# Kernel tuning notes

Measured on AMD Instinct MI355X. Metric: run time of the kernel, lower is better.

## Reference

```python
import jax, jax.numpy as jnp
import numpy as np

B, N, M = 16, 4096, 1024
IN_C, OUT_C, D = 6, 128, 64


def _gn(x, w, b, groups, eps=1e-5):
    # GroupNorm over (C//groups, L) per group; x: [B, C, L]
    Bb, C, L = x.shape
    xg = x.reshape(Bb, groups, C // groups, L)
    mu = xg.mean(axis=(2, 3), keepdims=True)
    var = xg.var(axis=(2, 3), keepdims=True)
    xn = ((xg - mu) * jax.lax.rsqrt(var + eps)).reshape(Bb, C, L)
    return xn * w[None, :, None] + b[None, :, None]


def _sa(xq, xkv, xyz_q, xyz_kv, qk_w, v_w, v_b, t_w, t_b, gn_w, gn_b, p_w, pg_w):
    # offset self-attention (PCT SA_Layer), q/k share weights
    pq = jnp.einsum('bcn,dc->bnd', xyz_q, p_w)              # [B,N,D]
    pk = jnp.einsum('bcm,dc->bdm', xyz_kv, pg_w)            # [B,D,M]
    q = jnp.einsum('bcn,dc->bnd', xq, qk_w) + pq            # [B,N,D]
    k = jnp.einsum('bcm,dc->bdm', xkv, qk_w) + pk           # [B,D,M]
    v = jnp.einsum('bcm,dc->bdm', xkv, v_w) + v_b[None, :, None] + pk
    attn = jax.nn.softmax(jnp.einsum('bnd,bdm->bnm', q, k), axis=-1)
    attn = attn / (1e-9 + attn.sum(axis=1, keepdims=True))  # L1 renorm over queries
    x_r = jnp.einsum('bnm,bdm->bnd', attn, v)               # [B,N,D]
    t = jnp.einsum('bnd,od->bon', q - x_r, t_w) + t_b[None, :, None]
    t = jax.nn.relu(_gn(t, gn_w, gn_b, 4))
    return jnp.swapaxes(q, 1, 2) + t                        # [B,D,N]


def _forward(x, x_global, xyz, xyz_global, conv1_w, gn1_w, gn1_b, conv2_w, gn2_w, gn2_b, sa_qk_w, sa_v_w, sa_v_b, sa_trans_w, sa_trans_b, sa_gn_w, sa_gn_b, sa_pos_w, sa_posG_w, fuse_w, fuse_gn_w, fuse_gn_b, convs1_w, convs1_b, gns1_w, gns1_b, convs2_w, convs2_b, gns2_w, gns2_b):
    h = jax.nn.relu(_gn(jnp.einsum('bcn,oc->bon', x, conv1_w), gn1_w, gn1_b, 16))
    hg = jax.nn.relu(_gn(jnp.einsum('bcm,oc->bom', x_global, conv2_w), gn2_w, gn2_b, 16))
    outs = []
    cur = h
    for i in range(4):
        cur = _sa(cur, hg, xyz, xyz_global, sa_qk_w[i], sa_v_w[i], sa_v_b[i],
                  sa_trans_w[i], sa_trans_b[i], sa_gn_w[i], sa_gn_b[i],
                  sa_pos_w[i], sa_posG_w[i])
        outs.append(cur)
    xc = jnp.concatenate(outs, axis=1)                      # [B,4D,N]
    xf = jax.nn.leaky_relu(_gn(jnp.einsum('bcn,oc->bon', xc, fuse_w), fuse_gn_w, fuse_gn_b, 16), 0.2)
    s1 = jax.nn.relu(_gn(jnp.einsum('bcn,oc->bon', xf, convs1_w) + convs1_b[None, :, None], gns1_w, gns1_b, 8))
    # dropout is identity in eval mode
    s2 = jax.nn.relu(_gn(jnp.einsum('bcn,oc->bon', s1, convs2_w) + convs2_b[None, :, None], gns2_w, gns2_b, 4))
    return jnp.swapaxes(s2, 1, 2)                           # [B,N,OUT_C]


def setup_inputs() -> dict:
    ks = jax.random.split(jax.random.key(0), 16)
    f = lambda k, s, sc=0.1: jax.random.normal(k, s, dtype=jnp.float32) * sc
    return {
        'x': f(ks[0], (B, IN_C, N), 1.0),
        'x_global': f(ks[1], (B, 32, M), 1.0),
        'xyz': f(ks[2], (B, 3, N), 1.0),
        'xyz_global': f(ks[3], (B, 3, M), 1.0),
        'conv1_w': f(ks[4], (D, IN_C)),
        'gn1_w': jnp.ones((D,), jnp.float32), 'gn1_b': jnp.zeros((D,), jnp.float32),
        'conv2_w': f(ks[5], (D, 32)),
        'gn2_w': jnp.ones((D,), jnp.float32), 'gn2_b': jnp.zeros((D,), jnp.float32),
        'sa_qk_w': f(ks[6], (4, D, D)),
        'sa_v_w': f(ks[7], (4, D, D)),
        'sa_v_b': jnp.zeros((4, D), jnp.float32),
        'sa_trans_w': f(ks[8], (4, D, D)),
        'sa_trans_b': jnp.zeros((4, D), jnp.float32),
        'sa_gn_w': jnp.ones((4, D), jnp.float32), 'sa_gn_b': jnp.zeros((4, D), jnp.float32),
        'sa_pos_w': f(ks[9], (4, D, 3)),
        'sa_posG_w': f(ks[10], (4, D, 3)),
        'fuse_w': f(ks[11], (2 * D, 4 * D)),
        'fuse_gn_w': jnp.ones((2 * D,), jnp.float32), 'fuse_gn_b': jnp.zeros((2 * D,), jnp.float32),
        'convs1_w': f(ks[12], (512, 2 * D)),
        'convs1_b': jnp.zeros((512,), jnp.float32),
        'gns1_w': jnp.ones((512,), jnp.float32), 'gns1_b': jnp.zeros((512,), jnp.float32),
        'convs2_w': f(ks[13], (OUT_C, 512)),
        'convs2_b': jnp.zeros((OUT_C,), jnp.float32),
        'gns2_w': jnp.ones((OUT_C,), jnp.float32), 'gns2_b': jnp.zeros((OUT_C,), jnp.float32),
    }


def reference(x, x_global, xyz, xyz_global, conv1_w, gn1_w, gn1_b, conv2_w, gn2_w, gn2_b, sa_qk_w, sa_v_w, sa_v_b, sa_trans_w, sa_trans_b, sa_gn_w, sa_gn_b, sa_pos_w, sa_posG_w, fuse_w, fuse_gn_w, fuse_gn_b, convs1_w, convs1_b, gns1_w, gns1_b, convs2_w, convs2_b, gns2_w, gns2_b):
    return _forward(x, x_global, xyz, xyz_global, conv1_w, gn1_w, gn1_b, conv2_w, gn2_w, gn2_b, sa_qk_w, sa_v_w, sa_v_b, sa_trans_w, sa_trans_b, sa_gn_w, sa_gn_b, sa_pos_w, sa_posG_w, fuse_w, fuse_gn_w, fuse_gn_b, convs1_w, convs1_b, gns1_w, gns1_b, convs2_w, convs2_b, gns2_w, gns2_b)
```

## Files before the change

### kernel.cpp

```cpp
#include <hip/hip_runtime.h>
#include <hip/hip_bf16.h>

namespace {

constexpr int BB = 16;
constexpr int NN = 4096;
constexpr int MM = 1024;

using f32x4  = __attribute__((ext_vector_type(4))) float;
using bf16x8 = __attribute__((ext_vector_type(8))) short;

__device__ __forceinline__ float actf(float x, int act) {
    if (act == 1) return fmaxf(x, 0.f);
    if (act == 2) return x >= 0.f ? x : 0.2f * x;
    return x;
}

__device__ __forceinline__ ushort f2bf(float x) {
    __hip_bfloat16 h = __float2bfloat16(x);
    return *reinterpret_cast<ushort*>(&h);
}

__device__ __forceinline__ uint hilo_pack(float x) {
    ushort h = f2bf(x);
    float hf = __uint_as_float(((uint)h) << 16);
    ushort l = f2bf(x - hf);
    return (uint)h | ((uint)l << 16);
}

__device__ __forceinline__ void split8(const uint* d, bf16x8& hi, bf16x8& lo) {
    union { uint u[4]; bf16x8 v; } H, L;
#pragma unroll
    for (int j = 0; j < 4; ++j) {
        H.u[j] = (d[2 * j] & 0xffffu) | (d[2 * j + 1] << 16);
        L.u[j] = (d[2 * j] >> 16) | (d[2 * j + 1] & 0xffff0000u);
    }
    hi = H.v; lo = L.v;
}

__global__ __launch_bounds__(256)
void conv_mfma(const float* __restrict__ X, int C, long x_bs,
               const float* __restrict__ W,
               const float* __restrict__ X2, long x2_bs,
               const float* __restrict__ W2,
               const float* __restrict__ bias,
               float* __restrict__ Y, long y_bs, int L)
{
    __shared__ uint Wp[64 * 33];
    __shared__ uint Xp[128 * 33];
    const int t  = threadIdx.x;
    const int b  = blockIdx.z;
    const int o0 = blockIdx.y * 64;
    const int l0 = blockIdx.x * 128;
    const int w  = t >> 6;
    const int ln = t & 15;
    const int lq = (t >> 4) & 3;
    const int wo = (w & 1) * 32;
    const int wl = (w >> 1) * 64;
    const int sl  = t & 127;
    const int sch = (t >> 7) * 16;

    f32x4 acc[2][4];
#pragma unroll
    for (int i = 0; i < 2; ++i)
#pragma unroll
        for (int j = 0; j < 4; ++j) acc[i][j] = (f32x4){0.f, 0.f, 0.f, 0.f};

    for (int c0 = 0; c0 < C; c0 += 32) {
        __syncthreads();
#pragma unroll
        for (int i = 0; i < 2; ++i) {
            int f = i * 256 + t;
            int r = f >> 3, q4 = (f & 7) * 4;
            float4 wv = *reinterpret_cast<const float4*>(&W[(long)(o0 + r) * C + c0 + q4]);
            Wp[r * 33 + q4 + 0] = hilo_pack(wv.x);
            Wp[r * 33 + q4 + 1] = hilo_pack(wv.y);
            Wp[r * 33 + q4 + 2] = hilo_pack(wv.z);
            Wp[r * 33 + q4 + 3] = hilo_pack(wv.w);
        }
        {
            const float* xc = X + (long)b * x_bs + (long)(c0 + sch) * L + l0 + sl;
            uint tmp[16];
#pragma unroll
            for (int c = 0; c < 16; ++c) tmp[c] = hilo_pack(xc[(long)c * L]);
#pragma unroll
            for (int c4 = 0; c4 < 4; ++c4) {
                uint4 v = make_uint4(tmp[c4 * 4], tmp[c4 * 4 + 1],
                                     tmp[c4 * 4 + 2], tmp[c4 * 4 + 3]);
                *reinterpret_cast<uint4*>(&Xp[sl * 33 + sch + c4 * 4]) = v;
            }
        }
        __syncthreads();

        bf16x8 ahi[2], alo[2];
#pragma unroll
        for (int ot = 0; ot < 2; ++ot) {
            uint d[8];
            *reinterpret_cast<uint4*>(d) =
                *reinterpret_cast<const uint4*>(&Wp[(wo + ot * 16 + ln) * 33 + lq * 8]);
            *reinterpret_cast<uint4*>(d + 4) =
                *reinterpret_cast<const uint4*>(&Wp[(wo + ot * 16 + ln) * 33 + lq * 8 + 4]);
            split8(d, ahi[ot], alo[ot]);
        }
#pragma unroll
        for (int lt = 0; lt < 4; ++lt) {
            uint d[8];
            *reinterpret_cast<uint4*>(d) =
                *reinterpret_cast<const uint4*>(&Xp[(wl + lt * 16 + ln) * 33 + lq * 8]);
            *reinterpret_cast<uint4*>(d + 4) =
                *reinterpret_cast<const uint4*>(&Xp[(wl + lt * 16 + ln) * 33 + lq * 8 + 4]);
            bf16x8 bhi, blo;
            split8(d, bhi, blo);
#pragma unroll
            for (int ot = 0; ot < 2; ++ot) {
                acc[ot][lt] = __builtin_amdgcn_mfma_f32_16x16x32_bf16(alo[ot], bhi, acc[ot][lt], 0, 0, 0);
                acc[ot][lt] = __builtin_amdgcn_mfma_f32_16x16x32_bf16(ahi[ot], blo, acc[ot][lt], 0, 0, 0);
                acc[ot][lt] = __builtin_amdgcn_mfma_f32_16x16x32_bf16(ahi[ot], bhi, acc[ot][lt], 0, 0, 0);
            }
        }
    }

    float x2v[4][3];
    if (X2) {
#pragma unroll
        for (int lt = 0; lt < 4; ++lt) {
            const int l = l0 + wl + lt * 16 + ln;
#pragma unroll
            for (int c = 0; c < 3; ++c)
                x2v[lt][c] = X2[(long)b * x2_bs + (long)c * L + l];
        }
    }
#pragma unroll
    for (int ot = 0; ot < 2; ++ot)
#pragma unroll
        for (int r = 0; r < 4; ++r) {
            const int o = o0 + wo + ot * 16 + lq * 4 + r;
            float base = bias ? bias[o] : 0.f;
            float w20 = 0.f, w21 = 0.f, w22 = 0.f;
            if (X2) {
                w20 = W2[o * 3 + 0];
                w21 = W2[o * 3 + 1];
                w22 = W2[o * 3 + 2];
            }
#pragma unroll
            for (int lt = 0; lt < 4; ++lt) {
                const int l = l0 + wl + lt * 16 + ln;
                float val = acc[ot][lt][r] + base;
                if (X2)
                    val += w20 * x2v[lt][0] + w21 * x2v[lt][1] + w22 * x2v[lt][2];
                Y[(long)b * y_bs + (long)o * L + l] = val;
            }
        }
}

__global__ __launch_bounds__(256)
void conv_gemm(const float* __restrict__ X1, int C1, long x1_bs,
               const float* __restrict__ W1,
               const float* __restrict__ X2, int C2, long x2_bs,
               const float* __restrict__ W2,
               const float* __restrict__ bias,
               float* __restrict__ Y, long y_bs, int L)
{
    __shared__ float Wt[64][17];
    __shared__ float Xt[16][128];
    const int t  = threadIdx.x;
    const int b  = blockIdx.z;
    const int o0 = blockIdx.y * 64;
    const int l0 = blockIdx.x * 128;
    const int ty = t >> 4, tx = t & 15;

    float acc[4][8];
#pragma unroll
    for (int i = 0; i < 4; ++i)
#pragma unroll
        for (int j = 0; j < 8; ++j) acc[i][j] = 0.f;

    for (int pass = 0; pass < 2; ++pass) {
        const float* X = pass ? X2 : X1;
        const float* W = pass ? W2 : W1;
        const int    C = pass ? C2 : C1;
        const long xbs = pass ? x2_bs : x1_bs;
        if (C <= 0 || X == nullptr) continue;
        for (int c0 = 0; c0 < C; c0 += 16) {
            __syncthreads();
#pragma unroll
            for (int i = 0; i < 4; ++i) {
                int flat = i * 256 + t;
                int oo = flat >> 4, kk = flat & 15;
                Wt[oo][kk] = (c0 + kk < C) ? W[(long)(o0 + oo) * C + c0 + kk] : 0.f;
            }
#pragma unroll
            for (int i = 0; i < 2; ++i) {
                int f4 = i * 256 + t;
                int kk = f4 >> 5, c4 = f4 & 31;
                float4 xv = make_float4(0.f, 0.f, 0.f, 0.f);
                if (c0 + kk < C)
                    xv = *reinterpret_cast<const float4*>(
                        X + (long)b * xbs + (long)(c0 + kk) * L + l0 + c4 * 4);
                *reinterpret_cast<float4*>(&Xt[kk][c4 * 4]) = xv;
            }
            __syncthreads();
#pragma unroll
            for (int kk = 0; kk < 16; ++kk) {
                float wv[4];
#pragma unroll
                for (int i = 0; i < 4; ++i) wv[i] = Wt[ty * 4 + i][kk];
                float4 xa = *reinterpret_cast<const float4*>(&Xt[kk][tx * 8]);
                float4 xb = *reinterpret_cast<const float4*>(&Xt[kk][tx * 8 + 4]);
                float xv[8] = {xa.x, xa.y, xa.z, xa.w, xb.x, xb.y, xb.z, xb.w};
#pragma unroll
                for (int i = 0; i < 4; ++i)
#pragma unroll
                    for (int j = 0; j < 8; ++j) acc[i][j] += wv[i] * xv[j];
            }
        }
    }

#pragma unroll
    for (int i = 0; i < 4; ++i) {
        const int oo = o0 + ty * 4 + i;
        const float bv = bias ? bias[oo] : 0.f;
        float* yp = Y + (long)b * y_bs + (long)oo * L + l0 + tx * 8;
        float4 v0 = make_float4(acc[i][0] + bv, acc[i][1] + bv, acc[i][2] + bv, acc[i][3] + bv);
        float4 v1 = make_float4(acc[i][4] + bv, acc[i][5] + bv, acc[i][6] + bv, acc[i][7] + bv);
        *reinterpret_cast<float4*>(yp)     = v0;
        *reinterpret_cast<float4*>(yp + 4) = v1;
    }
}

__global__ __launch_bounds__(256)
void gn_stats(const float* __restrict__ Y, long y_bs, int cpg, int L, int G,
              float* __restrict__ stats)
{
    const int bg = blockIdx.x;
    const int b = bg / G, g = bg - b * G;
    const float* p = Y + (long)b * y_bs + (long)g * cpg * L;
    const long cnt = (long)cpg * L;
    float s = 0.f, ss = 0.f;
    for (long i = (long)threadIdx.x * 4; i < cnt; i += 256 * 4) {
        float4 v = *reinterpret_cast<const float4*>(p + i);
        s  += v.x + v.y + v.z + v.w;
        ss += v.x * v.x + v.y * v.y + v.z * v.z + v.w * v.w;
    }
    __shared__ float rs[256], rss[256];
    rs[threadIdx.x] = s; rss[threadIdx.x] = ss;
    __syncthreads();
    for (int st = 128; st > 0; st >>= 1) {
        if (threadIdx.x < st) {
            rs[threadIdx.x]  += rs[threadIdx.x + st];
            rss[threadIdx.x] += rss[threadIdx.x + st];
        }
        __syncthreads();
    }
    if (threadIdx.x == 0) {
        float mu  = rs[0] / (float)cnt;
        float var = rss[0] / (float)cnt - mu * mu;
        stats[bg * 2]     = mu;
        stats[bg * 2 + 1] = rsqrtf(var + 1e-5f);
    }
}

__global__ __launch_bounds__(256)
void gn_apply(const float* __restrict__ src, long s_bs,
              float* __restrict__ dst, long d_bs,
              const float* __restrict__ res, long r_bs,
              const float* __restrict__ w, const float* __restrict__ bb,
              const float* __restrict__ stats,
              int C, int cpg, int L, int act)
{
    const long total4 = (long)BB * C * L / 4;
    const int G = C / cpg;
    for (long i4 = (long)blockIdx.x * 256 + threadIdx.x; i4 < total4;
         i4 += (long)gridDim.x * 256) {
        long flat = i4 * 4;
        int b = (int)(flat / ((long)C * L));
        long rem = flat - (long)b * C * L;
        int c = (int)(rem / L);
        long li = rem - (long)c * L;
        int sidx = (b * G + c / cpg) * 2;
        float mu = stats[sidx], rsig = stats[sidx + 1];
        float sc = rsig * w[c];
        float sh = bb[c] - mu * sc;
        float4 vv = *reinterpret_cast<const float4*>(src + (long)b * s_bs + (long)c * L + li);
        float4 ov;
        ov.x = actf(vv.x * sc + sh, act);
        ov.y = actf(vv.y * sc + sh, act);
        ov.z = actf(vv.z * sc + sh, act);
        ov.w = actf(vv.w * sc + sh, act);
        if (res) {
            float4 rv = *reinterpret_cast<const float4*>(res + (long)b * r_bs + (long)c * L + li);
            ov.x += rv.x; ov.y += rv.y; ov.z += rv.z; ov.w += rv.w;
        }
        *reinterpret_cast<float4*>(dst + (long)b * d_bs + (long)c * L + li) = ov;
    }
}

__global__ __launch_bounds__(256)
void tcvt(const float* __restrict__ in, ushort* __restrict__ out, int L)
{
    __shared__ float ls[64][65];
    const int t = threadIdx.x, b = blockIdx.y;
    const int l0 = blockIdx.x * 64;
#pragma unroll
    for (int i = 0; i < 16; ++i) {
        int f = i * 256 + t;
        int d = f >> 6, l = f & 63;
        ls[d][l] = in[(long)b * 64 * L + (long)d * L + l0 + l];
    }
    __syncthreads();
#pragma unroll
    for (int i = 0; i < 16; ++i) {
        int f = i * 256 + t;
        int l = f >> 6, d = f & 63;
        out[((long)b * L + l0 + l) * 64 + d] = f2bf(ls[d][l]);
    }
}

__global__ __launch_bounds__(256)
void attn_stats_mfma(const ushort* __restrict__ qt, const ushort* __restrict__ kt,
                     float* __restrict__ rowmax, float* __restrict__ rowinv,
                     float* __restrict__ csp)
{
    __shared__ float red[16][5];
    __shared__ float rs_mx[16], rs_inv[16];

    const int t  = threadIdx.x;
    const int b  = blockIdx.y;
    const int n0 = blockIdx.x * 16;
    const int w  = t >> 6;
    const int ln = t & 15;
    const int lq = (t >> 4) & 3;

    const ushort* qtb = qt + ((long)b * NN + n0) * 64;
    const ushort* ktb = kt + (long)b * MM * 64;

    bf16x8 aq[2];
#pragma unroll
    for (int ks = 0; ks < 2; ++ks)
        aq[ks] = *reinterpret_cast<const bf16x8*>(qtb + (long)ln * 64 + ks * 32 + lq * 8);

    f32x4 sc[16];
#pragma unroll
    for (int ib = 0; ib < 4; ++ib) {
        bf16x8 bk[4][2];
#pragma unroll
        for (int ii = 0; ii < 4; ++ii) {
            const int m0 = (w * 16 + ib * 4 + ii) * 16;
#pragma unroll
            for (int ks = 0; ks < 2; ++ks)
                bk[ii][ks] = *reinterpret_cast<const bf16x8*>(
                    ktb + (long)(m0 + ln) * 64 + ks * 32 + lq * 8);
        }
#pragma unroll
        for (int ii = 0; ii < 4; ++ii) {
            f32x4 acc = {0.f, 0.f, 0.f, 0.f};
            acc = __builtin_amdgcn_mfma_f32_16x16x32_bf16(aq[0], bk[ii][0], acc, 0, 0, 0);
            acc = __builtin_amdgcn_mfma_f32_16x16x32_bf16(aq[1], bk[ii][1], acc, 0, 0, 0);
            sc[ib * 4 + ii] = acc;
        }
    }

    float m4[4];
#pragma unroll
    for (int r = 0; r < 4; ++r) {
        float mx = sc[0][r];
#pragma unroll
        for (int i = 1; i < 16; ++i) mx = fmaxf(mx, sc[i][r]);
#pragma unroll
        for (int off = 1; off <= 8; off <<= 1) mx = fmaxf(mx, __shfl_xor(mx, off, 64));
        m4[r] = mx;
    }
    if (ln == 0)
#pragma unroll
        for (int r = 0; r < 4; ++r) red[lq * 4 + r][w] = m4[r];
    __syncthreads();
    if (t < 16) {
        float mx = fmaxf(fmaxf(red[t][0], red[t][1]), fmaxf(red[t][2], red[t][3]));
        rs_mx[t] = mx;
        rowmax[(long)b * NN + n0 + t] = mx;
    }
    __syncthreads();

    float mxr[4], s4[4];
#pragma unroll
    for (int r = 0; r < 4; ++r) { mxr[r] = rs_mx[lq * 4 + r]; s4[r] = 0.f; }
#pragma unroll
    for (int i = 0; i < 16; ++i)
#pragma unroll
        for (int r = 0; r < 4; ++r) {
            float e = __expf(sc[i][r] - mxr[r]);
            sc[i][r] = e;
            s4[r] += e;
        }
#pragma unroll
    for (int r = 0; r < 4; ++r)
#pragma unroll
        for (int off = 1; off <= 8; off <<= 1) s4[r] += __shfl_xor(s4[r], off, 64);
    if (ln == 0)
#pragma unroll
        for (int r = 0; r < 4; ++r) red[lq * 4 + r][w] = s4[r];
    __syncthreads();
    if (t < 16) {
        float es = red[t][0] + red[t][1] + red[t][2] + red[t][3];
        float inv = 1.0f / es;
        rs_inv[t] = inv;
        rowinv[(long)b * NN + n0 + t] = inv;
    }
    __syncthreads();

    float riv[4];
#pragma unroll
    for (int r = 0; r < 4; ++r) riv[r] = rs_inv[lq * 4 + r];
    const long cbase = ((long)b * (NN / 16) + blockIdx.x) * MM;
#pragma unroll
    for (int i = 0; i < 16; ++i) {
        float c = sc[i][0] * riv[0] + sc[i][1] * riv[1] + sc[i][2] * riv[2] + sc[i][3] * riv[3];
        c += __shfl_xor(c, 16, 64);
        c += __shfl_xor(c, 32, 64);
        if (lq == 0) csp[cbase + (w * 16 + i) * 16 + ln] = c;
    }
}

__global__ __launch_bounds__(256)
void attn_pv_mfma(const ushort* __restrict__ qt, const ushort* __restrict__ kt,
                  const ushort* __restrict__ vb,
                  const float* __restrict__ rowmax, const float* __restrict__ rowinv,
                  const float* __restrict__ qg, float* __restrict__ ug)
{
    __shared__ ushort Pb[2][32 * 256];

    const int t  = threadIdx.x;
    const int b  = blockIdx.y;
    const int n0 = blockIdx.x * 32;
    const int w  = t >> 6;
    const int rt = w & 1;
    const int ms = w >> 1;
    const int ln = t & 15;
    const int lq = (t >> 4) & 3;
    const int d0 = w * 16;

    const ushort* qtb = qt + ((long)b * NN + n0 + rt * 16) * 64;
    const ushort* ktb = kt + (long)b * MM * 64;
    const ushort* vbb = vb + (long)b * 64 * MM;

    float mx[4], ri[4];
#pragma unroll
    for (int r = 0; r < 4; ++r) {
        mx[r] = rowmax[(long)b * NN + n0 + rt * 16 + lq * 4 + r];
        ri[r] = rowinv[(long)b * NN + n0 + rt * 16 + lq * 4 + r];
    }

    bf16x8 aq[2];
#pragma unroll
    for (int ks = 0; ks < 2; ++ks)
        aq[ks] = *reinterpret_cast<const bf16x8*>(qtb + (long)ln * 64 + ks * 32 + lq * 8);

    f32x4 acc2[2];
    acc2[0] = (f32x4){0.f, 0.f, 0.f, 0.f};
    acc2[1] = (f32x4){0.f, 0.f, 0.f, 0.f};

    const int swz = (ln & 7) << 3;

    for (int c = 0; c < 4; ++c) {
        bf16x8 bk[8][2];
#pragma unroll
        for (int it = 0; it < 8; ++it) {
            const int m = c * 256 + ms * 128 + it * 16 + ln;
#pragma unroll
            for (int ks = 0; ks < 2; ++ks)
                bk[it][ks] = *reinterpret_cast<const bf16x8*>(
                    ktb + (long)m * 64 + ks * 32 + lq * 8);
        }
        ushort* pc = &Pb[c & 1][0];
#pragma unroll
        for (int it = 0; it < 8; ++it) {
            f32x4 acc = {0.f, 0.f, 0.f, 0.f};
            acc = __builtin_amdgcn_mfma_f32_16x16x32_bf16(aq[0], bk[it][0], acc, 0, 0, 0);
            acc = __builtin_amdgcn_mfma_f32_16x16x32_bf16(aq[1], bk[it][1], acc, 0, 0, 0);
            const int mc = ms * 128 + it * 16 + ln;
#pragma unroll
            for (int r = 0; r < 4; ++r) {
                const int n = rt * 16 + lq * 4 + r;
                float p = __expf(acc[r] - mx[r]) * ri[r];
                pc[n * 256 + (mc ^ ((n & 7) << 3))] = f2bf(p);
            }
        }
        __syncthreads();
#pragma unroll
        for (int ks = 0; ks < 8; ++ks) {
            bf16x8 av = *reinterpret_cast<const bf16x8*>(
                vbb + (long)(d0 + ln) * MM + c * 256 + ks * 32 + lq * 8);
            const int mo = ks * 32 + lq * 8;
#pragma unroll
            for (int nt = 0; nt < 2; ++nt) {
                bf16x8 bp = *reinterpret_cast<const bf16x8*>(
                    &pc[(nt * 16 + ln) * 256 + (mo ^ swz)]);
                acc2[nt] = __builtin_amdgcn_mfma_f32_16x16x32_bf16(av, bp, acc2[nt], 0, 0, 0);
            }
        }
    }

    const long qb = (long)b * 64 * NN;
#pragma unroll
    for (int nt = 0; nt < 2; ++nt)
#pragma unroll
        for (int r = 0; r < 4; ++r) {
            const int dd = d0 + lq * 4 + r;
            const long idx = qb + (long)dd * NN + n0 + nt * 16 + ln;
            ug[idx] = qg[idx] - acc2[nt][r];
        }
}

__global__ __launch_bounds__(256)
void colsum_reduce(const float* __restrict__ csp, float* __restrict__ cs, int NT)
{
    int idx = blockIdx.x * 256 + threadIdx.x;
    int b = idx / MM, m = idx - b * MM;
    const float* p = csp + (long)b * NT * MM + m;
    float s = 0.f;
    for (int i = 0; i < NT; ++i) s += p[(long)i * MM];
    cs[idx] = s;
}

__global__ __launch_bounds__(256)
void vscale_cvt(const float* __restrict__ v, const float* __restrict__ cs,
                ushort* __restrict__ vb)
{
    long i4 = (long)blockIdx.x * 256 + threadIdx.x;
    long flat = i4 * 4;
    int b = (int)(flat / (64L * MM));
    int m = (int)(flat % MM);
    float4 vv = *reinterpret_cast<const float4*>(v + flat);
    float4 cv = *reinterpret_cast<const float4*>(cs + (long)b * MM + m);
    ushort4 o;
    o.x = f2bf(vv.x / (1e-9f + cv.x));
    o.y = f2bf(vv.y / (1e-9f + cv.y));
    o.z = f2bf(vv.z / (1e-9f + cv.z));
    o.w = f2bf(vv.w / (1e-9f + cv.w));
    *reinterpret_cast<ushort4*>(vb + flat) = o;
}

__global__ __launch_bounds__(256)
void gn_out_transpose(const float* __restrict__ s2,
                      const float* __restrict__ w, const float* __restrict__ bb,
                      const float* __restrict__ stats,
                      float* __restrict__ out)
{
    __shared__ float ls[128 * 65];
    const int t = threadIdx.x;
    const int b = blockIdx.y;
    const int n0 = blockIdx.x * 64;
#pragma unroll
    for (int i = 0; i < 8; ++i) {
        int f4 = i * 256 + t;
        int o = f4 >> 4, c4 = f4 & 15;
        float4 vv = *reinterpret_cast<const float4*>(
            s2 + (long)b * 128 * NN + (long)o * NN + n0 + c4 * 4);
        int sidx = (b * 4 + (o >> 5)) * 2;
        float mu = stats[sidx], rsig = stats[sidx + 1];
        float sc = rsig * w[o], sh = bb[o] - mu * sc;
        ls[o * 65 + c4 * 4 + 0] = fmaxf(vv.x * sc + sh, 0.f);
        ls[o * 65 + c4 * 4 + 1] = fmaxf(vv.y * sc + sh, 0.f);
        ls[o * 65 + c4 * 4 + 2] = fmaxf(vv.z * sc + sh, 0.f);
        ls[o * 65 + c4 * 4 + 3] = fmaxf(vv.w * sc + sh, 0.f);
    }
    __syncthreads();
#pragma unroll
    for (int i = 0; i < 8; ++i) {
        int f4 = i * 256 + t;
        int nn = f4 >> 5, o4 = f4 & 31;
        float4 ov;
        ov.x = ls[(o4 * 4 + 0) * 65 + nn];
        ov.y = ls[(o4 * 4 + 1) * 65 + nn];
        ov.z = ls[(o4 * 4 + 2) * 65 + nn];
        ov.w = ls[(o4 * 4 + 3) * 65 + nn];
        *reinterpret_cast<float4*>(out + (long)b * NN * 128 + (long)(n0 + nn) * 128 + o4 * 4) = ov;
    }
}

}

extern "C" void kernel_launch(void* const* d_in, const int* in_sizes, int n_in,
                              void* d_out, int out_size, void* d_ws, size_t ws_size,
                              hipStream_t stream)
{
    (void)in_sizes; (void)n_in; (void)out_size; (void)ws_size;

    const float* x         = (const float*)d_in[0];
    const float* x_global  = (const float*)d_in[1];
    const float* xyz       = (const float*)d_in[2];
    const float* xyz_g     = (const float*)d_in[3];
    const float* conv1_w   = (const float*)d_in[4];
    const float* gn1_w     = (const float*)d_in[5];
    const float* gn1_b     = (const float*)d_in[6];
    const float* conv2_w   = (const float*)d_in[7];
    const float* gn2_w     = (const float*)d_in[8];
    const float* gn2_b     = (const float*)d_in[9];
    const float* sa_qk_w   = (const float*)d_in[10];
    const float* sa_v_w    = (const float*)d_in[11];
    const float* sa_v_b    = (const float*)d_in[12];
    const float* sa_t_w    = (const float*)d_in[13];
    const float* sa_t_b    = (const float*)d_in[14];
    const float* sa_gn_w   = (const float*)d_in[15];
    const float* sa_gn_b   = (const float*)d_in[16];
    const float* sa_pos_w  = (const float*)d_in[17];
    const float* sa_posG_w = (const float*)d_in[18];
    const float* fuse_w    = (const float*)d_in[19];
    const float* fuse_gn_w = (const float*)d_in[20];
    const float* fuse_gn_b = (const float*)d_in[21];
    const float* convs1_w  = (const float*)d_in[22];
    const float* convs1_b  = (const float*)d_in[23];
    const float* gns1_w    = (const float*)d_in[24];
    const float* gns1_b    = (const float*)d_in[25];
    const float* convs2_w  = (const float*)d_in[26];
    const float* convs2_b  = (const float*)d_in[27];
    const float* gns2_w    = (const float*)d_in[28];
    const float* gns2_b    = (const float*)d_in[29];

    constexpr long SZ_BN  = (long)BB * 64 * NN;
    constexpr long SZ_BM  = (long)BB * 64 * MM;
    constexpr long SZ_CSP = (long)BB * (NN / 16) * MM;

    float* ws = (float*)d_ws;
    long o = 0;
    float* p_h   = ws + o; o += SZ_BN;
    float* p_hg  = ws + o; o += SZ_BM;
    float* p_q   = ws + o; o += SZ_BN;
    float* p_k   = ws + o; o += SZ_BM;
    float* p_v   = ws + o; o += SZ_BM;
    float* p_u   = ws + o; o += SZ_BN;
    float* p_csp = ws + o; o += SZ_CSP;
    float* p_cs  = ws + o; o += (long)BB * MM;
    float* p_xc  = ws + o; o += (long)BB * 256 * NN;
    float* p_xf  = ws + o; o += (long)BB * 128 * NN;
    float* p_st  = ws + o; o += 4096;
    float* p_rmx = ws + o; o += (long)BB * NN;
    float* p_rin = ws + o; o += (long)BB * NN;
    float* p_s1  = ws;
    float* p_s2  = p_xf;
    ushort* p_qt = (ushort*)p_xf;
    ushort* p_kt = (ushort*)(p_xf + 2097152);
    ushort* p_vb = (ushort*)(p_xf + 2097152 + 524288);

    conv_gemm<<<dim3(NN / 128, 1, BB), 256, 0, stream>>>(
        x, 6, 6L * NN, conv1_w, nullptr, 0, 0, nullptr, nullptr, p_h, 64L * NN, NN);
    gn_stats<<<BB * 16, 256, 0, stream>>>(p_h, 64L * NN, 4, NN, 16, p_st);
    gn_apply<<<2048, 256, 0, stream>>>(p_h, 64L * NN, p_h, 64L * NN, nullptr, 0,
                                       gn1_w, gn1_b, p_st, 64, 4, NN, 1);
    conv_mfma<<<dim3(MM / 128, 1, BB), 256, 0, stream>>>(
        x_global, 32, 32L * MM, conv2_w, nullptr, 0, nullptr, nullptr, p_hg, 64L * MM, MM);
    gn_stats<<<BB * 16, 256, 0, stream>>>(p_hg, 64L * MM, 4, MM, 16, p_st);
    gn_apply<<<2048, 256, 0, stream>>>(p_hg, 64L * MM, p_hg, 64L * MM, nullptr, 0,
                                       gn2_w, gn2_b, p_st, 64, 4, MM, 1);

    const float* cur = p_h;
    long cur_bs = 64L * NN;
    for (int i = 0; i < 4; ++i) {
        conv_mfma<<<dim3(NN / 128, 1, BB), 256, 0, stream>>>(
            cur, 64, cur_bs, sa_qk_w + i * 4096,
            xyz, 3L * NN, sa_pos_w + i * 192, nullptr, p_q, 64L * NN, NN);
        tcvt<<<dim3(NN / 64, BB), 256, 0, stream>>>(p_q, p_qt, NN);
        conv_mfma<<<dim3(MM / 128, 1, BB), 256, 0, stream>>>(
            p_hg, 64, 64L * MM, sa_qk_w + i * 4096,
            xyz_g, 3L * MM, sa_posG_w + i * 192, nullptr, p_k, 64L * MM, MM);
        tcvt<<<dim3(MM / 64, BB), 256, 0, stream>>>(p_k, p_kt, MM);
        conv_mfma<<<dim3(MM / 128, 1, BB), 256, 0, stream>>>(
            p_hg, 64, 64L * MM, sa_v_w + i * 4096,
            xyz_g, 3L * MM, sa_posG_w + i * 192, sa_v_b + i * 64, p_v, 64L * MM, MM);
        attn_stats_mfma<<<dim3(NN / 16, BB), 256, 0, stream>>>(p_qt, p_kt, p_rmx, p_rin, p_csp);
        colsum_reduce<<<BB * MM / 256, 256, 0, stream>>>(p_csp, p_cs, NN / 16);
        vscale_cvt<<<BB * 64 * MM / 1024, 256, 0, stream>>>(p_v, p_cs, p_vb);
        attn_pv_mfma<<<dim3(NN / 32, BB), 256, 0, stream>>>(
            p_qt, p_kt, p_vb, p_rmx, p_rin, p_q, p_u);
        conv_mfma<<<dim3(NN / 128, 1, BB), 256, 0, stream>>>(
            p_u, 64, 64L * NN, sa_t_w + i * 4096,
            nullptr, 0, nullptr, sa_t_b + i * 64, p_h, 64L * NN, NN);
        gn_stats<<<BB * 4, 256, 0, stream>>>(p_h, 64L * NN, 16, NN, 4, p_st);
        gn_apply<<<2048, 256, 0, stream>>>(p_h, 64L * NN,
                                           p_xc + (long)i * 64 * NN, 256L * NN,
                                           p_q, 64L * NN,
                                           sa_gn_w + i * 64, sa_gn_b + i * 64, p_st,
                                           64, 16, NN, 1);
        cur = p_xc + (long)i * 64 * NN;
        cur_bs = 256L * NN;
    }

    conv_mfma<<<dim3(NN / 128, 2, BB), 256, 0, stream>>>(
        p_xc, 256, 256L * NN, fuse_w, nullptr, 0, nullptr, nullptr, p_xf, 128L * NN, NN);
    gn_stats<<<BB * 16, 256, 0, stream>>>(p_xf, 128L * NN, 8, NN, 16, p_st);
    gn_apply<<<2048, 256, 0, stream>>>(p_xf, 128L * NN, p_xf, 128L * NN, nullptr, 0,
                                       fuse_gn_w, fuse_gn_b, p_st, 128, 8, NN, 2);
    conv_mfma<<<dim3(NN / 128, 8, BB), 256, 0, stream>>>(
        p_xf, 128, 128L * NN, convs1_w, nullptr, 0, nullptr, convs1_b, p_s1, 512L * NN, NN);
    gn_stats<<<BB * 8, 256, 0, stream>>>(p_s1, 512L * NN, 64, NN, 8, p_st);
    gn_apply<<<2048, 256, 0, stream>>>(p_s1, 512L * NN, p_s1, 512L * NN, nullptr, 0,
                                       gns1_w, gns1_b, p_st, 512, 64, NN, 1);
    conv_mfma<<<dim3(NN / 128, 2, BB), 256, 0, stream>>>(
        p_s1, 512, 512L * NN, convs2_w, nullptr, 0, nullptr, convs2_b, p_s2, 128L * NN, NN);
    gn_stats<<<BB * 4, 256, 0, stream>>>(p_s2, 128L * NN, 32, NN, 4, p_st);
    gn_out_transpose<<<dim3(NN / 64, BB), 256, 0, stream>>>(
        p_s2, gns2_w, gns2_b, p_st, (float*)d_out);
}
```

Measured before the change: 1.582 ms.

## Fold GroupNorm apply into consumer conv loads and fuse bf16 transpose into conv epilogue

The separate gn_apply passes for h, hg, xf and s1 are removed. The normalization and activation are now applied on the fly when the next conv_mfma loads its input, using per-channel scale and shift precomputed in shared memory. The tcvt transpose kernels are dropped: conv_mfma writes the bf16 transposed copy (qt/kt) directly in its epilogue. The V operand loads in attn_pv are also hoisted ahead of the P computation. This trades several full read/write passes over large activations for extra arithmetic in loaders and recomputation of hg normalization in the K and V convs on every iteration.

```diff
diff --git a/kernel.cpp b/kernel.cpp
--- a/kernel.cpp
+++ b/kernel.cpp
@@ -44,10 +44,14 @@
                const float* __restrict__ X2, long x2_bs,
                const float* __restrict__ W2,
                const float* __restrict__ bias,
-               float* __restrict__ Y, long y_bs, int L)
+               const float* __restrict__ gnw, const float* __restrict__ gnb,
+               const float* __restrict__ gstats, int cpg, int act,
+               float* __restrict__ Y, long y_bs, int L,
+               ushort* __restrict__ Yt)
 {
     __shared__ uint Wp[64 * 33];
     __shared__ uint Xp[128 * 33];
+    __shared__ float scs[512], shs[512];
     const int t  = threadIdx.x;
     const int b  = blockIdx.z;
     const int o0 = blockIdx.y * 64;
@@ -60,6 +64,16 @@
     const int sl  = t & 127;
     const int sch = (t >> 7) * 16;
 
+    if (gnw) {
+        for (int c = t; c < C; c += 256) {
+            int sidx = (b * (C / cpg) + c / cpg) * 2;
+            float mu = gstats[sidx], rs = gstats[sidx + 1];
+            float sc = rs * gnw[c];
+            scs[c] = sc;
+            shs[c] = gnb[c] - mu * sc;
+        }
+    }
+
     f32x4 acc[2][4];
 #pragma unroll
     for (int i = 0; i < 2; ++i)
@@ -80,9 +94,21 @@
         }
         {
             const float* xc = X + (long)b * x_bs + (long)(c0 + sch) * L + l0 + sl;
+            float scr[16], shr[16];
+            if (gnw) {
+#pragma unroll
+                for (int c = 0; c < 16; ++c) {
+                    scr[c] = scs[c0 + sch + c];
+                    shr[c] = shs[c0 + sch + c];
+                }
+            }
             uint tmp[16];
 #pragma unroll
-            for (int c = 0; c < 16; ++c) tmp[c] = hilo_pack(xc[(long)c * L]);
+            for (int c = 0; c < 16; ++c) {
+                float xv = xc[(long)c * L];
+                if (gnw) xv = actf(xv * scr[c] + shr[c], act);
+                tmp[c] = hilo_pack(xv);
+            }
 #pragma unroll
             for (int c4 = 0; c4 < 4; ++c4) {
                 uint4 v = make_uint4(tmp[c4 * 4], tmp[c4 * 4 + 1],
@@ -131,26 +157,37 @@
         }
     }
 #pragma unroll
-    for (int ot = 0; ot < 2; ++ot)
+    for (int ot = 0; ot < 2; ++ot) {
+        float bb4[4], w20[4], w21[4], w22[4];
 #pragma unroll
         for (int r = 0; r < 4; ++r) {
             const int o = o0 + wo + ot * 16 + lq * 4 + r;
-            float base = bias ? bias[o] : 0.f;
-            float w20 = 0.f, w21 = 0.f, w22 = 0.f;
+            bb4[r] = bias ? bias[o] : 0.f;
             if (X2) {
-                w20 = W2[o * 3 + 0];
-                w21 = W2[o * 3 + 1];
-                w22 = W2[o * 3 + 2];
-            }
-#pragma unroll
-            for (int lt = 0; lt < 4; ++lt) {
-                const int l = l0 + wl + lt * 16 + ln;
-                float val = acc[ot][lt][r] + base;
+                w20[r] = W2[o * 3 + 0];
+                w21[r] = W2[o * 3 + 1];
+                w22[r] = W2[o * 3 + 2];
+            }
+        }
+#pragma unroll
+        for (int lt = 0; lt < 4; ++lt) {
+            const int l = l0 + wl + lt * 16 + ln;
+            float fv[4];
+#pragma unroll
+            for (int r = 0; r < 4; ++r) {
+                float val = acc[ot][lt][r] + bb4[r];
                 if (X2)
-                    val += w20 * x2v[lt][0] + w21 * x2v[lt][1] + w22 * x2v[lt][2];
-                Y[(long)b * y_bs + (long)o * L + l] = val;
-            }
-        }
+                    val += w20[r] * x2v[lt][0] + w21[r] * x2v[lt][1] + w22[r] * x2v[lt][2];
+                fv[r] = val;
+                Y[(long)b * y_bs + (long)(o0 + wo + ot * 16 + lq * 4 + r) * L + l] = val;
+            }
+            if (Yt) {
+                ushort4 o4 = make_ushort4(f2bf(fv[0]), f2bf(fv[1]), f2bf(fv[2]), f2bf(fv[3]));
+                *reinterpret_cast<ushort4*>(
+                    &Yt[((long)b * L + l) * 64 + wo + ot * 16 + lq * 4]) = o4;
+            }
+        }
+    }
 }
 
 __global__ __launch_bounds__(256)
@@ -296,27 +333,6 @@
 }
 
 __global__ __launch_bounds__(256)
-void tcvt(const float* __restrict__ in, ushort* __restrict__ out, int L)
-{
-    __shared__ float ls[64][65];
-    const int t = threadIdx.x, b = blockIdx.y;
-    const int l0 = blockIdx.x * 64;
-#pragma unroll
-    for (int i = 0; i < 16; ++i) {
-        int f = i * 256 + t;
-        int d = f >> 6, l = f & 63;
-        ls[d][l] = in[(long)b * 64 * L + (long)d * L + l0 + l];
-    }
-    __syncthreads();
-#pragma unroll
-    for (int i = 0; i < 16; ++i) {
-        int f = i * 256 + t;
-        int l = f >> 6, d = f & 63;
-        out[((long)b * L + l0 + l) * 64 + d] = f2bf(ls[d][l]);
-    }
-}
-
-__global__ __launch_bounds__(256)
 void attn_stats_mfma(const ushort* __restrict__ qt, const ushort* __restrict__ kt,
                      float* __restrict__ rowmax, float* __restrict__ rowinv,
                      float* __restrict__ csp)
@@ -471,6 +487,12 @@
                 bk[it][ks] = *reinterpret_cast<const bf16x8*>(
                     ktb + (long)m * 64 + ks * 32 + lq * 8);
         }
+        bf16x8 av[8];
+#pragma unroll
+        for (int ks = 0; ks < 8; ++ks)
+            av[ks] = *reinterpret_cast<const bf16x8*>(
+                vbb + (long)(d0 + ln) * MM + c * 256 + ks * 32 + lq * 8);
+
         ushort* pc = &Pb[c & 1][0];
 #pragma unroll
         for (int it = 0; it < 8; ++it) {
@@ -488,14 +510,12 @@
         __syncthreads();
 #pragma unroll
         for (int ks = 0; ks < 8; ++ks) {
-            bf16x8 av = *reinterpret_cast<const bf16x8*>(
-                vbb + (long)(d0 + ln) * MM + c * 256 + ks * 32 + lq * 8);
             const int mo = ks * 32 + lq * 8;
 #pragma unroll
             for (int nt = 0; nt < 2; ++nt) {
                 bf16x8 bp = *reinterpret_cast<const bf16x8*>(
                     &pc[(nt * 16 + ln) * 256 + (mo ^ swz)]);
-                acc2[nt] = __builtin_amdgcn_mfma_f32_16x16x32_bf16(av, bp, acc2[nt], 0, 0, 0);
+                acc2[nt] = __builtin_amdgcn_mfma_f32_16x16x32_bf16(av[ks], bp, acc2[nt], 0, 0, 0);
             }
         }
     }
@@ -623,50 +643,57 @@
 
     float* ws = (float*)d_ws;
     long o = 0;
-    float* p_h   = ws + o; o += SZ_BN;
-    float* p_hg  = ws + o; o += SZ_BM;
-    float* p_q   = ws + o; o += SZ_BN;
-    float* p_k   = ws + o; o += SZ_BM;
-    float* p_v   = ws + o; o += SZ_BM;
-    float* p_u   = ws + o; o += SZ_BN;
-    float* p_csp = ws + o; o += SZ_CSP;
-    float* p_cs  = ws + o; o += (long)BB * MM;
-    float* p_xc  = ws + o; o += (long)BB * 256 * NN;
-    float* p_xf  = ws + o; o += (long)BB * 128 * NN;
-    float* p_st  = ws + o; o += 4096;
-    float* p_rmx = ws + o; o += (long)BB * NN;
-    float* p_rin = ws + o; o += (long)BB * NN;
-    float* p_s1  = ws;
-    float* p_s2  = p_xf;
+    float* p_h    = ws + o; o += SZ_BN;
+    float* p_hg   = ws + o; o += SZ_BM;
+    float* p_q    = ws + o; o += SZ_BN;
+    float* p_k    = ws + o; o += SZ_BM;
+    float* p_v    = ws + o; o += SZ_BM;
+    float* p_u    = ws + o; o += SZ_BN;
+    float* p_csp  = ws + o; o += SZ_CSP;
+    float* p_cs   = ws + o; o += (long)BB * MM;
+    float* p_xc   = ws + o; o += (long)BB * 256 * NN;
+    float* p_xf   = ws + o; o += (long)BB * 128 * NN;
+    float* p_st   = ws + o; o += 4096;
+    float* p_st_h = ws + o; o += 1024;
+    float* p_st_hg= ws + o; o += 1024;
+    float* p_st_xf= ws + o; o += 1024;
+    float* p_st_s1= ws + o; o += 1024;
+    float* p_rmx  = ws + o; o += (long)BB * NN;
+    float* p_rin  = ws + o; o += (long)BB * NN;
+    float* p_s1   = ws;
+    float* p_s2   = p_xf;
     ushort* p_qt = (ushort*)p_xf;
     ushort* p_kt = (ushort*)(p_xf + 2097152);
     ushort* p_vb = (ushort*)(p_xf + 2097152 + 524288);
 
     conv_gemm<<<dim3(NN / 128, 1, BB), 256, 0, stream>>>(
         x, 6, 6L * NN, conv1_w, nullptr, 0, 0, nullptr, nullptr, p_h, 64L * NN, NN);
-    gn_stats<<<BB * 16, 256, 0, stream>>>(p_h, 64L * NN, 4, NN, 16, p_st);
-    gn_apply<<<2048, 256, 0, stream>>>(p_h, 64L * NN, p_h, 64L * NN, nullptr, 0,
-                                       gn1_w, gn1_b, p_st, 64, 4, NN, 1);
+    gn_stats<<<BB * 16, 256, 0, stream>>>(p_h, 64L * NN, 4, NN, 16, p_st_h);
     conv_mfma<<<dim3(MM / 128, 1, BB), 256, 0, stream>>>(
-        x_global, 32, 32L * MM, conv2_w, nullptr, 0, nullptr, nullptr, p_hg, 64L * MM, MM);
-    gn_stats<<<BB * 16, 256, 0, stream>>>(p_hg, 64L * MM, 4, MM, 16, p_st);
-    gn_apply<<<2048, 256, 0, stream>>>(p_hg, 64L * MM, p_hg, 64L * MM, nullptr, 0,
-                                       gn2_w, gn2_b, p_st, 64, 4, MM, 1);
+        x_global, 32, 32L * MM, conv2_w, nullptr, 0, nullptr, nullptr,
+        nullptr, nullptr, nullptr, 1, 0, p_hg, 64L * MM, MM, nullptr);
+    gn_stats<<<BB * 16, 256, 0, stream>>>(p_hg, 64L * MM, 4, MM, 16, p_st_hg);
 
     const float* cur = p_h;
     long cur_bs = 64L * NN;
     for (int i = 0; i < 4; ++i) {
+        const bool fold0 = (i == 0);
         conv_mfma<<<dim3(NN / 128, 1, BB), 256, 0, stream>>>(
-            cur, 64, cur_bs, sa_qk_w + i * 4096,
-            xyz, 3L * NN, sa_pos_w + i * 192, nullptr, p_q, 64L * NN, NN);
-        tcvt<<<dim3(NN / 64, BB), 256, 0, stream>>>(p_q, p_qt, NN);
+            cur, fold0 ? 64 : 64, cur_bs, sa_qk_w + i * 4096,
+            xyz, 3L * NN, sa_pos_w + i * 192, nullptr,
+            fold0 ? gn1_w : nullptr, fold0 ? gn1_b : nullptr,
+            fold0 ? p_st_h : nullptr, 4, 1,
+            p_q, 64L * NN, NN, p_qt);
         conv_mfma<<<dim3(MM / 128, 1, BB), 256, 0, stream>>>(
             p_hg, 64, 64L * MM, sa_qk_w + i * 4096,
-            xyz_g, 3L * MM, sa_posG_w + i * 192, nullptr, p_k, 64L * MM, MM);
-        tcvt<<<dim3(MM / 64, BB), 256, 0, stream>>>(p_k, p_kt, MM);
+            xyz_g, 3L * MM, sa_posG_w + i * 192, nullptr,
+            gn2_w, gn2_b, p_st_hg, 4, 1,
+            p_k, 64L * MM, MM, p_kt);
         conv_mfma<<<dim3(MM / 128, 1, BB), 256, 0, stream>>>(
             p_hg, 64, 64L * MM, sa_v_w + i * 4096,
-            xyz_g, 3L * MM, sa_posG_w + i * 192, sa_v_b + i * 64, p_v, 64L * MM, MM);
+            xyz_g, 3L * MM, sa_posG_w + i * 192, sa_v_b + i * 64,
+            gn2_w, gn2_b, p_st_hg, 4, 1,
+            p_v, 64L * MM, MM, nullptr);
         attn_stats_mfma<<<dim3(NN / 16, BB), 256, 0, stream>>>(p_qt, p_kt, p_rmx, p_rin, p_csp);
         colsum_reduce<<<BB * MM / 256, 256, 0, stream>>>(p_csp, p_cs, NN / 16);
         vscale_cvt<<<BB * 64 * MM / 1024, 256, 0, stream>>>(p_v, p_cs, p_vb);
@@ -674,7 +701,9 @@
             p_qt, p_kt, p_vb, p_rmx, p_rin, p_q, p_u);
         conv_mfma<<<dim3(NN / 128, 1, BB), 256, 0, stream>>>(
             p_u, 64, 64L * NN, sa_t_w + i * 4096,
-            nullptr, 0, nullptr, sa_t_b + i * 64, p_h, 64L * NN, NN);
+            nullptr, 0, nullptr, sa_t_b + i * 64,
+            nullptr, nullptr, nullptr, 1, 0,
+            p_h, 64L * NN, NN, nullptr);
         gn_stats<<<BB * 4, 256, 0, stream>>>(p_h, 64L * NN, 16, NN, 4, p_st);
         gn_apply<<<2048, 256, 0, stream>>>(p_h, 64L * NN,
                                            p_xc + (long)i * 64 * NN, 256L * NN,
@@ -686,17 +715,16 @@
     }
 
     conv_mfma<<<dim3(NN / 128, 2, BB), 256, 0, stream>>>(
-        p_xc, 256, 256L * NN, fuse_w, nullptr, 0, nullptr, nullptr, p_xf, 128L * NN, NN);
-    gn_stats<<<BB * 16, 256, 0, stream>>>(p_xf, 128L * NN, 8, NN, 16, p_st);
-    gn_apply<<<2048, 256, 0, stream>>>(p_xf, 128L * NN, p_xf, 128L * NN, nullptr, 0,
-                                       fuse_gn_w, fuse_gn_b, p_st, 128, 8, NN, 2);
+        p_xc, 256, 256L * NN, fuse_w, nullptr, 0, nullptr, nullptr,
+        nullptr, nullptr, nullptr, 1, 0, p_xf, 128L * NN, NN, nullptr);
+    gn_stats<<<BB * 16, 256, 0, stream>>>(p_xf, 128L * NN, 8, NN, 16, p_st_xf);
     conv_mfma<<<dim3(NN / 128, 8, BB), 256, 0, stream>>>(
-        p_xf, 128, 128L * NN, convs1_w, nullptr, 0, nullptr, convs1_b, p_s1, 512L * NN, NN);
-    gn_stats<<<BB * 8, 256, 0, stream>>>(p_s1, 512L * NN, 64, NN, 8, p_st);
-    gn_apply<<<2048, 256, 0, stream>>>(p_s1, 512L * NN, p_s1, 512L * NN, nullptr, 0,
-                                       gns1_w, gns1_b, p_st, 512, 64, NN, 1);
+        p_xf, 128, 128L * NN, convs1_w, nullptr, 0, nullptr, convs1_b,
+        fuse_gn_w, fuse_gn_b, p_st_xf, 8, 2, p_s1, 512L * NN, NN, nullptr);
+    gn_stats<<<BB * 8, 256, 0, stream>>>(p_s1, 512L * NN, 64, NN, 8, p_st_s1);
     conv_mfma<<<dim3(NN / 128, 2, BB), 256, 0, stream>>>(
-        p_s1, 512, 512L * NN, convs2_w, nullptr, 0, nullptr, convs2_b, p_s2, 128L * NN, NN);
+        p_s1, 512, 512L * NN, convs2_w, nullptr, 0, nullptr, convs2_b,
+        gns1_w, gns1_b, p_st_s1, 64, 1, p_s2, 128L * NN, NN, nullptr);
     gn_stats<<<BB * 4, 256, 0, stream>>>(p_s2, 128L * NN, 32, NN, 4, p_st);
     gn_out_transpose<<<dim3(NN / 64, BB), 256, 0, stream>>>(
         p_s2, gns2_w, gns2_b, p_st, (float*)d_out);
```

Result: slower. 1.830 ms (+15.7%).
